# Kernel optimization log

Hardware: AMD Instinct MI355X
Metric: run time of the kernel (lower is better)

Reference implementation:

```python
import jax, jax.numpy as jnp
import numpy as np
import math

B, S, H, Dh, Dr, HID, C = 2, 2048, 16, 128, 64, 2048, 512

def _linear(x, w, b):
    return x @ w.T + b

def _rope(x):
    # x: [B, H, S, Dr]; interleaved-pair rotation as in the torch module
    d = x.shape[-1]
    s = x.shape[2]
    inv_freq = 1.0 / (10000.0 ** (jnp.arange(0, d, 2, dtype=jnp.float32) / d))
    sinusoid = jnp.arange(s, dtype=jnp.float32)[:, None] * inv_freq[None, :]  # [S, d/2]
    sin, cos = jnp.sin(sinusoid), jnp.cos(sinusoid)  # broadcast over B,H
    x1 = x[..., 0::2]
    x2 = x[..., 1::2]
    rot = jnp.stack([x1 * cos - x2 * sin, x1 * sin + x2 * cos], axis=-1)
    return rot.reshape(x.shape)

def setup_inputs() -> dict:
    key = jax.random.key(0)
    ks = jax.random.split(key, 9)
    sc = 0.02
    return {
        "x": jax.random.normal(ks[0], (B, S, HID), jnp.float32),
        "d_kv_w": jax.random.normal(ks[1], (C, HID), jnp.float32) * sc,
        "d_kv_b": jnp.zeros((C,), jnp.float32),
        "u_k_w": jax.random.normal(ks[2], (H * Dh, C), jnp.float32) * sc,
        "u_k_b": jnp.zeros((H * Dh,), jnp.float32),
        "u_v_w": jax.random.normal(ks[3], (H * Dh, C), jnp.float32) * sc,
        "u_v_b": jnp.zeros((H * Dh,), jnp.float32),
        "d_q_w": jax.random.normal(ks[4], (C, HID), jnp.float32) * sc,
        "d_q_b": jnp.zeros((C,), jnp.float32),
        "u_q_w": jax.random.normal(ks[5], (H * Dh, C), jnp.float32) * sc,
        "u_q_b": jnp.zeros((H * Dh,), jnp.float32),
        "qr_w": jax.random.normal(ks[6], (H * Dr, C), jnp.float32) * sc,
        "qr_b": jnp.zeros((H * Dr,), jnp.float32),
        "out_w": jax.random.normal(ks[7], (HID, H * Dh), jnp.float32) * sc,
        "out_b": jnp.zeros((HID,), jnp.float32),
    }

def reference(x, d_kv_w, d_kv_b, u_k_w, u_k_b, u_v_w, u_v_b,
              d_q_w, d_q_b, u_q_w, u_q_b, qr_w, qr_b, out_w, out_b):
    b, s, _ = x.shape
    kv_c = _linear(x, d_kv_w, d_kv_b)                      # [B,S,C]
    k_c = _linear(kv_c, u_k_w, u_k_b).reshape(b, s, H, Dh)
    k_r = _linear(kv_c, qr_w, qr_b).reshape(b, s, H, Dr)   # note: qr_proj reused, as in source
    v = _linear(kv_c, u_v_w, u_v_b).reshape(b, s, H, Dh)
    q_c_lat = _linear(x, d_q_w, d_q_b)                     # [B,S,C]
    q_c = _linear(q_c_lat, u_q_w, u_q_b).reshape(b, s, H, Dh)
    q_r = _linear(q_c_lat, qr_w, qr_b).reshape(b, s, H, Dr)
    # RoPE operates on [B,H,S,Dr]
    q_r = _rope(q_r.transpose(0, 2, 1, 3)).transpose(0, 2, 1, 3)
    k_r = _rope(k_r.transpose(0, 2, 1, 3)).transpose(0, 2, 1, 3)
    q = jnp.concatenate([q_c, q_r], axis=-1)               # [B,S,H,Dh+Dr]
    k = jnp.concatenate([k_c, k_r], axis=-1)
    scale = 1.0 / math.sqrt(Dh + Dr)
    scores = jnp.einsum('bqhd,bkhd->bhqk', q, k) * scale   # [B,H,S,S]
    probs = jax.nn.softmax(scores, axis=-1)
    ctx = jnp.einsum('bhqk,bkhd->bqhd', probs, v).reshape(b, s, H * Dh)
    return _linear(ctx, out_w, out_b)
```

## Files before the change

### kernel.cpp

```cpp
#include <hip/hip_runtime.h>
#include <hip/hip_bf16.h>
#include <math.h>
#include <stdint.h>

#define NB 2
#define NS 2048
#define NH 16
#define NDH 128
#define NDR 64
#define NHID 2048
#define NC 512

typedef unsigned short u16;
typedef short short8 __attribute__((ext_vector_type(8)));
typedef short short4v __attribute__((ext_vector_type(4)));
typedef float f32x4 __attribute__((ext_vector_type(4)));
typedef float f32x16 __attribute__((ext_vector_type(16)));
typedef int int2v __attribute__((ext_vector_type(2)));

template <int V> struct IC { static constexpr int value = V; };

__device__ __forceinline__ u16 f2bf(float f) {
  union { float f; uint32_t u; } c; c.f = f;
  uint32_t u = c.u + 0x7fffu + ((c.u >> 16) & 1u);
  return (u16)(u >> 16);
}
__device__ __forceinline__ void async16(const void* g, void* l) {
  __builtin_amdgcn_global_load_lds((const __attribute__((address_space(1))) void*)g,
                                   (__attribute__((address_space(3))) void*)l, 16, 0, 0);
}
__device__ __forceinline__ int cvtpk(float a, float b) {
  int r;
  asm("v_cvt_pk_bf16_f32 %0, %1, %2" : "=v"(r) : "v"(a), "v"(b));
  return r;
}
__device__ __forceinline__ void fsincos(float ang, float& sn, float& cs) {
  float rev = ang * 0.15915494309189535f;
  rev = rev - floorf(rev);
  float s, c;
  asm("v_sin_f32 %0, %1" : "=v"(s) : "v"(rev));
  asm("v_cos_f32 %0, %1" : "=v"(c) : "v"(rev));
  sn = s; cs = c;
}

struct CastArgs {
  const float* src[8];
  u16* dst[8];
  int start[8];
};

__global__ __launch_bounds__(256) void cast_kernel(CastArgs a) {
  int blk = blockIdx.x;
  int ti = 0;
#pragma unroll
  for (int i = 1; i < 8; ++i) ti += (blk >= a.start[i]) ? 1 : 0;
  size_t off = (size_t)(blk - a.start[ti]) * 2048 + (size_t)threadIdx.x * 8;
  const float4* s = (const float4*)(a.src[ti] + off);
  float4 v0 = s[0], v1 = s[1];
  u16 o[8];
  o[0] = f2bf(v0.x); o[1] = f2bf(v0.y); o[2] = f2bf(v0.z); o[3] = f2bf(v0.w);
  o[4] = f2bf(v1.x); o[5] = f2bf(v1.y); o[6] = f2bf(v1.z); o[7] = f2bf(v1.w);
  *(short8*)(a.dst[ti] + off) = *(short8*)o;
}

struct GemmSeg {
  const u16* A;
  const u16* W;
  const float* bias;
  void* dst;
  int K;
  int mode;
  int ldc;
};
struct GemmArgs {
  GemmSeg seg[5];
  int nbstart[6];
  int nseg;
};

template <int NW>
__global__ __launch_bounds__(NW * 64) void gemm_bt(GemmArgs ga) {
  constexpr int NT = NW * 64;
  constexpr int NJ = (NW == 8) ? 2 : 4;
  __shared__ char glds[32768];
  const int nb = blockIdx.x, mb = blockIdx.y;
  int si = 0;
  for (int i = 1; i < ga.nseg; ++i) si += (nb >= ga.nbstart[i]) ? 1 : 0;
  GemmSeg sg = ga.seg[si];
  const int nbl = nb - ga.nbstart[si];
  const int K = sg.K;
  const int t = threadIdx.x;
  const int l = t & 63, w = t >> 6;
  const int r0 = t >> 2, c0 = (t & 3) * 8;
  const int wm = (NW == 8 ? (w >> 2) : (w >> 1)) * 64;
  const int wn = (NW == 8) ? (w & 3) * 32 : (w & 1) * 64;
  const int frow = l & 15, fk = (l >> 4) * 8;
  const int lafO = ((wm + frow) * 32 + fk) * 2;
  const int lbfO = 8192 + ((wn + frow) * 32 + fk) * 2;

  const u16* apA = sg.A + (size_t)mb * 128 * K + (size_t)r0 * K + c0;
  const u16* wpA = sg.W + (size_t)nbl * 128 * K + (size_t)r0 * K + c0;

  auto stage = [&](int bufOff) {
    if constexpr (NT == 512) {
      async16(apA, glds + bufOff + t * 16);
      async16(wpA, glds + bufOff + 8192 + t * 16);
    } else {
      async16(apA, glds + bufOff + t * 16);
      async16(apA + (size_t)64 * K, glds + bufOff + 4096 + t * 16);
      async16(wpA, glds + bufOff + 8192 + t * 16);
      async16(wpA + (size_t)64 * K, glds + bufOff + 12288 + t * 16);
    }
    apA += 32; wpA += 32;
  };

  const f32x4 vzero = {0.f, 0.f, 0.f, 0.f};
  f32x4 acc[4][NJ];
#pragma unroll
  for (int i = 0; i < 4; ++i)
#pragma unroll
    for (int j = 0; j < NJ; ++j) acc[i][j] = vzero;

  stage(0);
  const int nk = K / 32;

  auto ktile = [&](auto bufc, bool stageNext) {
    constexpr int BO = decltype(bufc)::value;
    if (stageNext) {
      stage(BO ^ 16384);
      if constexpr (NT == 512)
        asm volatile("s_waitcnt vmcnt(2)" ::: "memory");
      else
        asm volatile("s_waitcnt vmcnt(4)" ::: "memory");
    } else {
      asm volatile("s_waitcnt vmcnt(0)" ::: "memory");
    }
    __builtin_amdgcn_s_barrier();
    asm volatile("" ::: "memory");
    short8 af[4], bfr[NJ];
#pragma unroll
    for (int i = 0; i < 4; ++i) af[i] = *(const short8*)(glds + BO + lafO + i * 1024);
#pragma unroll
    for (int j = 0; j < NJ; ++j) bfr[j] = *(const short8*)(glds + BO + lbfO + j * 1024);
    __builtin_amdgcn_s_setprio(1);
#pragma unroll
    for (int i = 0; i < 4; ++i)
#pragma unroll
      for (int j = 0; j < NJ; ++j)
        acc[i][j] = __builtin_amdgcn_mfma_f32_16x16x32_bf16(af[i], bfr[j], acc[i][j], 0, 0, 0);
    __builtin_amdgcn_s_setprio(0);
    asm volatile("s_waitcnt lgkmcnt(0)" ::: "memory");
    __builtin_amdgcn_s_barrier();
  };

  for (int kk = 0; kk < nk; kk += 2) {
    ktile(IC<0>{}, true);
    ktile(IC<16384>{}, kk + 2 < nk);
  }

  const int rb = (l >> 4) * 4;
  const int cl = l & 15;
  const int mode = sg.mode;
  if (mode == 0) {
    u16* D = (u16*)sg.dst;
#pragma unroll
    for (int i = 0; i < 4; ++i)
#pragma unroll
      for (int j = 0; j < NJ; ++j) {
        int col = nbl * 128 + wn + j * 16 + cl;
        float bv = sg.bias[col];
#pragma unroll
        for (int r = 0; r < 4; ++r) {
          int row = mb * 128 + wm + i * 16 + rb + r;
          D[(size_t)row * sg.ldc + col] = f2bf(acc[i][j][r] + bv);
        }
      }
  } else if (mode == 2) {
    float* D = (float*)sg.dst;
#pragma unroll
    for (int i = 0; i < 4; ++i)
#pragma unroll
      for (int j = 0; j < NJ; ++j) {
        int col = nbl * 128 + wn + j * 16 + cl;
        float bv = sg.bias[col];
#pragma unroll
        for (int r = 0; r < 4; ++r) {
          int row = mb * 128 + wm + i * 16 + rb + r;
          D[(size_t)row * sg.ldc + col] = acc[i][j][r] + bv;
        }
      }
  } else if (mode == 1) {
    u16* D = (u16*)sg.dst;
#pragma unroll
    for (int i = 0; i < 4; ++i) {
      int row0 = mb * 128 + wm + i * 16 + rb;
      int bb = row0 >> 11, s = row0 & (NS - 1);
#pragma unroll
      for (int j = 0; j < NJ; ++j) {
        int col = nbl * 128 + wn + j * 16 + cl;
        int hh = col >> 7, dv = col & 127;
        float bv = sg.bias[col];
        u16 pk[4];
#pragma unroll
        for (int r = 0; r < 4; ++r) pk[r] = f2bf(acc[i][j][r] + bv);
        size_t cell = ((size_t)((bb * NH + hh) * (NS / 8) + (s >> 3)) * 128 + dv) * 8 + (s & 7);
        *(short4v*)(D + cell) = *(short4v*)pk;
      }
    }
  } else if (mode == 4) {
    u16* D = (u16*)sg.dst;
#pragma unroll
    for (int i = 0; i < 4; ++i) {
      int row0 = mb * 128 + wm + i * 16 + rb;
      int bb = row0 >> 11, s = row0 & (NS - 1);
#pragma unroll
      for (int j = 0; j < NJ; ++j) {
        int col = nbl * 128 + wn + j * 16 + cl;
        int hh = col >> 7, d = col & 127;
        float bv = sg.bias[col];
        size_t base = ((size_t)((bb * NH + hh) * 24 + (d >> 3)) * NS + s) * 8 + (d & 7);
#pragma unroll
        for (int r = 0; r < 4; ++r) D[base + r * 8] = f2bf(acc[i][j][r] + bv);
      }
    }
  } else if (mode == 5) {
    u16* D = (u16*)sg.dst;
#pragma unroll
    for (int i = 0; i < 4; ++i) {
      int row0 = mb * 128 + wm + i * 16 + rb;
      int bb = row0 >> 11, s = row0 & (NS - 1);
#pragma unroll
      for (int j = 0; j < NJ; ++j) {
        int col = nbl * 128 + wn + j * 16 + cl;
        int hh = col >> 6, dr = col & 63;
        int jp = dr >> 1;
        bool ev = !(dr & 1);
        float invf = exp2f(-(float)jp * 0.41524101186f);
        float bv = sg.bias[col];
        size_t base = ((size_t)((bb * NH + hh) * 24 + 16 + (dr >> 3)) * NS + s) * 8 + (dr & 7);
#pragma unroll
        for (int r = 0; r < 4; ++r) {
          float v = acc[i][j][r] + bv;
          float p = __shfl_xor(v, 1);
          float sn, cs;
          fsincos((float)(s + r) * invf, sn, cs);
          float out = ev ? (v * cs - p * sn) : (p * sn + v * cs);
          D[base + r * 8] = f2bf(out);
        }
      }
    }
  } else {
    u16* D = (u16*)sg.dst;
#pragma unroll
    for (int i = 0; i < 4; ++i) {
      int row0 = mb * 128 + wm + i * 16 + rb;
      int s = row0 & (NS - 1);
#pragma unroll
      for (int j = 0; j < NJ; ++j) {
        int col = nbl * 128 + wn + j * 16 + cl;
        int dr = col & 63;
        int jp = dr >> 1;
        bool ev = !(dr & 1);
        float invf = exp2f(-(float)jp * 0.41524101186f);
        float bv = sg.bias[col];
#pragma unroll
        for (int r = 0; r < 4; ++r) {
          float v = acc[i][j][r] + bv;
          float p = __shfl_xor(v, 1);
          float sn, cs;
          fsincos((float)(s + r) * invf, sn, cs);
          float out = ev ? (v * cs - p * sn) : (p * sn + v * cs);
          D[(size_t)(row0 + r) * sg.ldc + col] = f2bf(out);
        }
      }
    }
  }
}

__global__ __launch_bounds__(256, 2) void attn_kernel(
    const u16* __restrict__ Qc, const u16* __restrict__ Qr,
    const u16* __restrict__ Ktb, const u16* __restrict__ Vtb,
    u16* __restrict__ Ctx) {
  extern __shared__ char smem[];
  const int t = threadIdx.x, w = t >> 6, l = t & 63;
  const int hi = l >> 5, q32 = l & 31;
  const int lin = blockIdx.x;
  const int xcd = lin & 7, idx = lin >> 3;
  const int bh = xcd * 4 + (idx >> 4);
  const int qb = idx & 15;
  const int b = bh >> 4, h = bh & 15;
  const int q0 = qb * 128 + w * 32;

  short8 qf[12];
  {
    const u16* qcp = Qc + ((size_t)(b * NS + q0 + q32)) * NHID + h * NDH + hi * 8;
    const u16* qrp = Qr + ((size_t)(b * NS + q0 + q32)) * (NH * NDR) + h * NDR + hi * 8;
#pragma unroll
    for (int dw = 0; dw < 8; ++dw) qf[dw] = *(const short8*)(qcp + dw * 16);
#pragma unroll
    for (int dw = 0; dw < 4; ++dw) qf[8 + dw] = *(const short8*)(qrp + dw * 16);
  }
#pragma unroll
  for (int dw = 0; dw < 12; ++dw) asm volatile("" :: "v"(qf[dw]));

  const int w2 = t >> 6;
  const u16* kp[6];
#pragma unroll
  for (int r = 0; r < 6; ++r)
    kp[r] = Ktb + ((size_t)(bh * 24 + r * 4 + w2) * NS + l) * 8;
  const u16* vp = Vtb + (size_t)bh * NS * 128 + t * 8;

  const int kbase = q32 * 16 + hi * 1024;
  const int vbase = 24576 + q32 * 16 + hi * 2048;

  float lsum = 0.f;
  f32x16 acc[4];
#pragma unroll
  for (int i = 0; i < 4; ++i)
#pragma unroll
    for (int r = 0; r < 16; ++r) acc[i][r] = 0.f;
  const float scale2 = 0.10411757f;

  auto stage_into = [&](int bufOff) {
#pragma unroll
    for (int r = 0; r < 6; ++r) { async16(kp[r], smem + bufOff + r * 4096 + t * 16); kp[r] += 512; }
#pragma unroll
    for (int r = 0; r < 4; ++r) async16(vp + r * 2048, smem + bufOff + 24576 + r * 4096 + t * 16);
    vp += 8192;
  };
  stage_into(0);

  auto pv_block = [&](const f32x16& sp, int n, const char* base) {
#pragma unroll
    for (int w2i = 0; w2i < 2; ++w2i) {
      const int bse = w2i * 8;
      int A0 = cvtpk(sp[bse + 0], sp[bse + 1]);
      int A1 = cvtpk(sp[bse + 2], sp[bse + 3]);
      int B0 = cvtpk(sp[bse + 4], sp[bse + 5]);
      int B1 = cvtpk(sp[bse + 6], sp[bse + 7]);
      int2v r02 = __builtin_amdgcn_permlane32_swap(A0, B0, false, false);
      int2v r13 = __builtin_amdgcn_permlane32_swap(A1, B1, false, false);
      union { int i[4]; short8 s; } F;
      F.i[0] = r02[0]; F.i[1] = r13[0]; F.i[2] = r02[1]; F.i[3] = r13[1];
      const int W = n * 2 + w2i;
      __builtin_amdgcn_s_setprio(1);
#pragma unroll
      for (int d32 = 0; d32 < 4; ++d32) {
        short8 va = *(const short8*)(base + W * 4096 + d32 * 512);
        acc[d32] = __builtin_amdgcn_mfma_f32_32x32x16_bf16(va, F.s, acc[d32], 0, 0, 0);
      }
      __builtin_amdgcn_s_setprio(0);
    }
  };

  auto tile = [&](auto bufc, bool stageNext) {
    constexpr int BO = decltype(bufc)::value;
    if (stageNext) {
      stage_into(BO ^ 40960);
      asm volatile("s_waitcnt vmcnt(10)" ::: "memory");
    } else {
      asm volatile("s_waitcnt vmcnt(0)" ::: "memory");
    }
    __builtin_amdgcn_s_barrier();
    asm volatile("" ::: "memory");

    f32x16 sa0, sa1;
#pragma unroll
    for (int r = 0; r < 16; ++r) { sa0[r] = 0.f; sa1[r] = 0.f; }
#pragma unroll
    for (int dw = 0; dw < 12; ++dw) {
      short8 k0 = *(const short8*)(smem + BO + kbase + dw * 2048);
      __builtin_amdgcn_s_setprio(1);
      sa0 = __builtin_amdgcn_mfma_f32_32x32x16_bf16(k0, qf[dw], sa0, 0, 0, 0);
      __builtin_amdgcn_s_setprio(0);
    }
#pragma unroll
    for (int dw = 0; dw < 12; ++dw) {
      short8 k1 = *(const short8*)(smem + BO + kbase + dw * 2048 + 512);
      __builtin_amdgcn_s_setprio(1);
      sa1 = __builtin_amdgcn_mfma_f32_32x32x16_bf16(k1, qf[dw], sa1, 0, 0, 0);
      __builtin_amdgcn_s_setprio(0);
    }
    float ps = 0.f;
#pragma unroll
    for (int r = 0; r < 16; ++r) {
      float p = exp2f(sa0[r] * scale2);
      sa0[r] = p;
      ps += p;
    }
    pv_block(sa0, 0, (const char*)smem + BO + vbase);
#pragma unroll
    for (int r = 0; r < 16; ++r) {
      float p = exp2f(sa1[r] * scale2);
      sa1[r] = p;
      ps += p;
    }
    pv_block(sa1, 1, (const char*)smem + BO + vbase);
    ps += __shfl_xor(ps, 32);
    lsum += ps;

    asm volatile("s_waitcnt lgkmcnt(0)" ::: "memory");
    __builtin_amdgcn_s_barrier();
  };

  for (int kv = 0; kv < NS / 64; kv += 2) {
    tile(IC<0>{}, true);
    tile(IC<40960>{}, kv + 2 < NS / 64);
  }

  float invq = 1.f / lsum;
  u16* dst = Ctx + ((size_t)(b * NS + q0 + q32)) * NHID + h * NDH + hi * 4;
#pragma unroll
  for (int d32 = 0; d32 < 4; ++d32)
#pragma unroll
    for (int m2x = 0; m2x < 4; ++m2x) {
      float a0 = acc[d32][m2x * 4 + 0] * invq, a1 = acc[d32][m2x * 4 + 1] * invq;
      float a2 = acc[d32][m2x * 4 + 2] * invq, a3 = acc[d32][m2x * 4 + 3] * invq;
      union { int i[2]; short4v s; } pu;
      pu.i[0] = cvtpk(a0, a1);
      pu.i[1] = cvtpk(a2, a3);
      *(short4v*)(dst + d32 * 32 + m2x * 8) = pu.s;
    }
}

extern "C" void kernel_launch(void* const* d_in, const int* in_sizes, int n_in,
                              void* d_out, int out_size, void* d_ws, size_t ws_size,
                              hipStream_t stream) {
  (void)in_sizes; (void)n_in; (void)out_size;
  const float* x      = (const float*)d_in[0];
  const float* d_kv_w = (const float*)d_in[1];
  const float* d_kv_b = (const float*)d_in[2];
  const float* u_k_w  = (const float*)d_in[3];
  const float* u_k_b  = (const float*)d_in[4];
  const float* u_v_w  = (const float*)d_in[5];
  const float* u_v_b  = (const float*)d_in[6];
  const float* d_q_w  = (const float*)d_in[7];
  const float* d_q_b  = (const float*)d_in[8];
  const float* u_q_w  = (const float*)d_in[9];
  const float* u_q_b  = (const float*)d_in[10];
  const float* qr_w   = (const float*)d_in[11];
  const float* qr_b   = (const float*)d_in[12];
  const float* out_w  = (const float*)d_in[13];
  const float* out_b  = (const float*)d_in[14];

  char* ws = (char*)d_ws;
  size_t off = 0;
  auto alloc = [&](size_t bytes) -> void* {
    void* p = ws + off;
    off += (bytes + 255) & ~(size_t)255;
    return p;
  };
  u16* xb   = (u16*)alloc((size_t)NB * NS * NHID * 2);
  u16* wdkv = (u16*)alloc((size_t)NC * NHID * 2);
  u16* wuk  = (u16*)alloc((size_t)NH * NDH * NC * 2);
  u16* wuv  = (u16*)alloc((size_t)NH * NDH * NC * 2);
  u16* wdq  = (u16*)alloc((size_t)NC * NHID * 2);
  u16* wuq  = (u16*)alloc((size_t)NH * NDH * NC * 2);
  u16* wqr  = (u16*)alloc((size_t)NH * NDR * NC * 2);
  u16* wout = (u16*)alloc((size_t)NHID * NH * NDH * 2);
  u16* kvc  = (u16*)alloc((size_t)NB * NS * NC * 2);
  u16* qlat = (u16*)alloc((size_t)NB * NS * NC * 2);
  u16* Ktb  = (u16*)alloc((size_t)NB * NH * 24 * NS * 8 * 2);
  u16* Vtb  = (u16*)alloc((size_t)NB * NH * NS * NDH * 2);
  u16* Qc   = (u16*)alloc((size_t)NB * NS * NH * NDH * 2);
  u16* Qrt  = (u16*)alloc((size_t)NB * NS * NH * NDR * 2);
  u16* ctx  = xb;
  if (off > ws_size) return;

  {
    CastArgs ca;
    const float* srcs[8] = {x, d_kv_w, u_k_w, u_v_w, d_q_w, u_q_w, qr_w, out_w};
    u16* dsts[8] = {xb, wdkv, wuk, wuv, wdq, wuq, wqr, wout};
    int sizes[8] = {NB * NS * NHID, NC * NHID, NH * NDH * NC, NH * NDH * NC,
                    NC * NHID, NH * NDH * NC, NH * NDR * NC, NHID * NH * NDH};
    int st = 0;
    for (int i = 0; i < 8; ++i) {
      ca.src[i] = srcs[i]; ca.dst[i] = dsts[i]; ca.start[i] = st;
      st += sizes[i] / 2048;
    }
    cast_kernel<<<dim3(st), dim3(256), 0, stream>>>(ca);
  }

  {
    GemmArgs ga;
    ga.nseg = 2;
    ga.seg[0] = {xb, wdkv, d_kv_b, kvc, NHID, 0, NC};
    ga.seg[1] = {xb, wdq,  d_q_b,  qlat, NHID, 0, NC};
    for (int i = 2; i < 5; ++i) ga.seg[i] = ga.seg[0];
    ga.nbstart[0] = 0; ga.nbstart[1] = 4; ga.nbstart[2] = 8;
    ga.nbstart[3] = 8; ga.nbstart[4] = 8; ga.nbstart[5] = 8;
    gemm_bt<8><<<dim3(8, 32), dim3(512), 0, stream>>>(ga);
  }

  {
    GemmArgs ga;
    ga.nseg = 5;
    ga.seg[0] = {kvc,  wuk, u_k_b, Ktb, NC, 4, 0};
    ga.seg[1] = {kvc,  wuv, u_v_b, Vtb, NC, 1, 0};
    ga.seg[2] = {kvc,  wqr, qr_b,  Ktb, NC, 5, 0};
    ga.seg[3] = {qlat, wuq, u_q_b, Qc,  NC, 0, NH * NDH};
    ga.seg[4] = {qlat, wqr, qr_b,  Qrt, NC, 3, NH * NDR};
    ga.nbstart[0] = 0;  ga.nbstart[1] = 16; ga.nbstart[2] = 32;
    ga.nbstart[3] = 40; ga.nbstart[4] = 56; ga.nbstart[5] = 64;
    gemm_bt<4><<<dim3(64, 32), dim3(256), 0, stream>>>(ga);
  }

  hipFuncSetAttribute((const void*)attn_kernel,
                      hipFuncAttributeMaxDynamicSharedMemorySize, 81920);
  attn_kernel<<<dim3(512), dim3(256), 81920, stream>>>(Qc, Qrt, Ktb, Vtb, ctx);

  {
    GemmArgs ga;
    ga.nseg = 1;
    ga.seg[0] = {ctx, wout, out_b, d_out, NHID, 2, NHID};
    for (int i = 1; i < 5; ++i) ga.seg[i] = ga.seg[0];
    ga.nbstart[0] = 0;
    for (int i = 1; i < 6; ++i) ga.nbstart[i] = 16;
    gemm_bt<4><<<dim3(16, 32), dim3(256), 0, stream>>>(ga);
  }
}
```

Before: 256.0 us.

## Widen GEMM tiles, fold softmax scale into Q, row-sum via MFMA

```diff
diff --git a/kernel.cpp b/kernel.cpp
--- a/kernel.cpp
+++ b/kernel.cpp
@@ -17,6 +17,8 @@
 typedef float f32x4 __attribute__((ext_vector_type(4)));
 typedef float f32x16 __attribute__((ext_vector_type(16)));
 typedef int int2v __attribute__((ext_vector_type(2)));
+
+#define SC2 0.10411757f
 
 template <int V> struct IC { static constexpr int value = V; };
 
@@ -71,6 +73,7 @@
   int K;
   int mode;
   int ldc;
+  float oscale;
 };
 struct GemmArgs {
   GemmSeg seg[5];
@@ -78,11 +81,12 @@
   int nseg;
 };
 
-template <int NW>
-__global__ __launch_bounds__(NW * 64) void gemm_bt(GemmArgs ga) {
-  constexpr int NT = NW * 64;
-  constexpr int NJ = (NW == 8) ? 2 : 4;
-  __shared__ char glds[32768];
+template <int BN>
+__global__ __launch_bounds__(512) void gemm_bt(GemmArgs ga) {
+  constexpr int NT = 512;
+  constexpr int NJ = BN / 64;
+  constexpr int BUF = 8192 + BN * 64;
+  __shared__ char glds[2 * BUF];
   const int nb = blockIdx.x, mb = blockIdx.y;
   int si = 0;
   for (int i = 1; i < ga.nseg; ++i) si += (nb >= ga.nbstart[i]) ? 1 : 0;
@@ -92,25 +96,20 @@
   const int t = threadIdx.x;
   const int l = t & 63, w = t >> 6;
   const int r0 = t >> 2, c0 = (t & 3) * 8;
-  const int wm = (NW == 8 ? (w >> 2) : (w >> 1)) * 64;
-  const int wn = (NW == 8) ? (w & 3) * 32 : (w & 1) * 64;
+  const int wm = (w >> 2) * 64;
+  const int wn = (w & 3) * (BN / 4);
   const int frow = l & 15, fk = (l >> 4) * 8;
   const int lafO = ((wm + frow) * 32 + fk) * 2;
   const int lbfO = 8192 + ((wn + frow) * 32 + fk) * 2;
 
   const u16* apA = sg.A + (size_t)mb * 128 * K + (size_t)r0 * K + c0;
-  const u16* wpA = sg.W + (size_t)nbl * 128 * K + (size_t)r0 * K + c0;
+  const u16* wpA = sg.W + (size_t)nbl * BN * K + (size_t)r0 * K + c0;
 
   auto stage = [&](int bufOff) {
-    if constexpr (NT == 512) {
-      async16(apA, glds + bufOff + t * 16);
-      async16(wpA, glds + bufOff + 8192 + t * 16);
-    } else {
-      async16(apA, glds + bufOff + t * 16);
-      async16(apA + (size_t)64 * K, glds + bufOff + 4096 + t * 16);
-      async16(wpA, glds + bufOff + 8192 + t * 16);
-      async16(wpA + (size_t)64 * K, glds + bufOff + 12288 + t * 16);
-    }
+    async16(apA, glds + bufOff + t * 16);
+    async16(wpA, glds + bufOff + 8192 + t * 16);
+    if constexpr (BN == 256)
+      async16(wpA + (size_t)128 * K, glds + bufOff + 16384 + t * 16);
     apA += 32; wpA += 32;
   };
 
@@ -127,11 +126,11 @@
   auto ktile = [&](auto bufc, bool stageNext) {
     constexpr int BO = decltype(bufc)::value;
     if (stageNext) {
-      stage(BO ^ 16384);
-      if constexpr (NT == 512)
+      stage(BO ^ BUF);
+      if constexpr (BN == 256)
+        asm volatile("s_waitcnt vmcnt(3)" ::: "memory");
+      else
         asm volatile("s_waitcnt vmcnt(2)" ::: "memory");
-      else
-        asm volatile("s_waitcnt vmcnt(4)" ::: "memory");
     } else {
       asm volatile("s_waitcnt vmcnt(0)" ::: "memory");
     }
@@ -155,7 +154,7 @@
 
   for (int kk = 0; kk < nk; kk += 2) {
     ktile(IC<0>{}, true);
-    ktile(IC<16384>{}, kk + 2 < nk);
+    ktile(IC<BUF>{}, kk + 2 < nk);
   }
 
   const int rb = (l >> 4) * 4;
@@ -163,16 +162,17 @@
   const int mode = sg.mode;
   if (mode == 0) {
     u16* D = (u16*)sg.dst;
+    float os = sg.oscale;
 #pragma unroll
     for (int i = 0; i < 4; ++i)
 #pragma unroll
       for (int j = 0; j < NJ; ++j) {
-        int col = nbl * 128 + wn + j * 16 + cl;
+        int col = nbl * BN + wn + j * 16 + cl;
         float bv = sg.bias[col];
 #pragma unroll
         for (int r = 0; r < 4; ++r) {
           int row = mb * 128 + wm + i * 16 + rb + r;
-          D[(size_t)row * sg.ldc + col] = f2bf(acc[i][j][r] + bv);
+          D[(size_t)row * sg.ldc + col] = f2bf((acc[i][j][r] + bv) * os);
         }
       }
   } else if (mode == 2) {
@@ -181,7 +181,7 @@
     for (int i = 0; i < 4; ++i)
 #pragma unroll
       for (int j = 0; j < NJ; ++j) {
-        int col = nbl * 128 + wn + j * 16 + cl;
+        int col = nbl * BN + wn + j * 16 + cl;
         float bv = sg.bias[col];
 #pragma unroll
         for (int r = 0; r < 4; ++r) {
@@ -197,7 +197,7 @@
       int bb = row0 >> 11, s = row0 & (NS - 1);
 #pragma unroll
       for (int j = 0; j < NJ; ++j) {
-        int col = nbl * 128 + wn + j * 16 + cl;
+        int col = nbl * BN + wn + j * 16 + cl;
         int hh = col >> 7, dv = col & 127;
         float bv = sg.bias[col];
         u16 pk[4];
@@ -215,7 +215,7 @@
       int bb = row0 >> 11, s = row0 & (NS - 1);
 #pragma unroll
       for (int j = 0; j < NJ; ++j) {
-        int col = nbl * 128 + wn + j * 16 + cl;
+        int col = nbl * BN + wn + j * 16 + cl;
         int hh = col >> 7, d = col & 127;
         float bv = sg.bias[col];
         size_t base = ((size_t)((bb * NH + hh) * 24 + (d >> 3)) * NS + s) * 8 + (d & 7);
@@ -231,7 +231,7 @@
       int bb = row0 >> 11, s = row0 & (NS - 1);
 #pragma unroll
       for (int j = 0; j < NJ; ++j) {
-        int col = nbl * 128 + wn + j * 16 + cl;
+        int col = nbl * BN + wn + j * 16 + cl;
         int hh = col >> 6, dr = col & 63;
         int jp = dr >> 1;
         bool ev = !(dr & 1);
@@ -251,13 +251,14 @@
     }
   } else {
     u16* D = (u16*)sg.dst;
+    float os = sg.oscale;
 #pragma unroll
     for (int i = 0; i < 4; ++i) {
       int row0 = mb * 128 + wm + i * 16 + rb;
       int s = row0 & (NS - 1);
 #pragma unroll
       for (int j = 0; j < NJ; ++j) {
-        int col = nbl * 128 + wn + j * 16 + cl;
+        int col = nbl * BN + wn + j * 16 + cl;
         int dr = col & 63;
         int jp = dr >> 1;
         bool ev = !(dr & 1);
@@ -270,7 +271,7 @@
           float sn, cs;
           fsincos((float)(s + r) * invf, sn, cs);
           float out = ev ? (v * cs - p * sn) : (p * sn + v * cs);
-          D[(size_t)(row0 + r) * sg.ldc + col] = f2bf(out);
+          D[(size_t)(row0 + r) * sg.ldc + col] = f2bf(out * os);
         }
       }
     }
@@ -313,13 +314,14 @@
   const int kbase = q32 * 16 + hi * 1024;
   const int vbase = 24576 + q32 * 16 + hi * 2048;
 
-  float lsum = 0.f;
-  f32x16 acc[4];
-#pragma unroll
-  for (int i = 0; i < 4; ++i)
-#pragma unroll
-    for (int r = 0; r < 16; ++r) acc[i][r] = 0.f;
-  const float scale2 = 0.10411757f;
+  f32x16 acc[4], accS, fz;
+#pragma unroll
+  for (int r = 0; r < 16; ++r) { fz[r] = 0.f; accS[r] = 0.f; }
+#pragma unroll
+  for (int i = 0; i < 4; ++i) acc[i] = fz;
+  union { int i[4]; short8 s; } ONES;
+  ONES.i[0] = 0x3F803F80; ONES.i[1] = 0x3F803F80;
+  ONES.i[2] = 0x3F803F80; ONES.i[3] = 0x3F803F80;
 
   auto stage_into = [&](int bufOff) {
 #pragma unroll
@@ -330,14 +332,18 @@
   };
   stage_into(0);
 
-  auto pv_block = [&](const f32x16& sp, int n, const char* base) {
+  auto pv_block = [&](const f32x16& s, int n, const char* vb) {
 #pragma unroll
     for (int w2i = 0; w2i < 2; ++w2i) {
       const int bse = w2i * 8;
-      int A0 = cvtpk(sp[bse + 0], sp[bse + 1]);
-      int A1 = cvtpk(sp[bse + 2], sp[bse + 3]);
-      int B0 = cvtpk(sp[bse + 4], sp[bse + 5]);
-      int B1 = cvtpk(sp[bse + 6], sp[bse + 7]);
+      float p0 = exp2f(s[bse + 0]), p1 = exp2f(s[bse + 1]);
+      float p2 = exp2f(s[bse + 2]), p3 = exp2f(s[bse + 3]);
+      float p4 = exp2f(s[bse + 4]), p5 = exp2f(s[bse + 5]);
+      float p6 = exp2f(s[bse + 6]), p7 = exp2f(s[bse + 7]);
+      int A0 = cvtpk(p0, p1);
+      int A1 = cvtpk(p2, p3);
+      int B0 = cvtpk(p4, p5);
+      int B1 = cvtpk(p6, p7);
       int2v r02 = __builtin_amdgcn_permlane32_swap(A0, B0, false, false);
       int2v r13 = __builtin_amdgcn_permlane32_swap(A1, B1, false, false);
       union { int i[4]; short8 s; } F;
@@ -346,9 +352,10 @@
       __builtin_amdgcn_s_setprio(1);
 #pragma unroll
       for (int d32 = 0; d32 < 4; ++d32) {
-        short8 va = *(const short8*)(base + W * 4096 + d32 * 512);
+        short8 va = *(const short8*)(vb + W * 4096 + d32 * 512);
         acc[d32] = __builtin_amdgcn_mfma_f32_32x32x16_bf16(va, F.s, acc[d32], 0, 0, 0);
       }
+      accS = __builtin_amdgcn_mfma_f32_32x32x16_bf16(ONES.s, F.s, accS, 0, 0, 0);
       __builtin_amdgcn_s_setprio(0);
     }
   };
@@ -365,39 +372,27 @@
     asm volatile("" ::: "memory");
 
     f32x16 sa0, sa1;
-#pragma unroll
-    for (int r = 0; r < 16; ++r) { sa0[r] = 0.f; sa1[r] = 0.f; }
-#pragma unroll
-    for (int dw = 0; dw < 12; ++dw) {
+    {
+      short8 k0 = *(const short8*)(smem + BO + kbase);
+      short8 k1 = *(const short8*)(smem + BO + kbase + 512);
+      __builtin_amdgcn_s_setprio(1);
+      sa0 = __builtin_amdgcn_mfma_f32_32x32x16_bf16(k0, qf[0], fz, 0, 0, 0);
+      sa1 = __builtin_amdgcn_mfma_f32_32x32x16_bf16(k1, qf[0], fz, 0, 0, 0);
+      __builtin_amdgcn_s_setprio(0);
+    }
+#pragma unroll
+    for (int dw = 1; dw < 12; ++dw) {
       short8 k0 = *(const short8*)(smem + BO + kbase + dw * 2048);
+      short8 k1 = *(const short8*)(smem + BO + kbase + dw * 2048 + 512);
       __builtin_amdgcn_s_setprio(1);
       sa0 = __builtin_amdgcn_mfma_f32_32x32x16_bf16(k0, qf[dw], sa0, 0, 0, 0);
-      __builtin_amdgcn_s_setprio(0);
-    }
-#pragma unroll
-    for (int dw = 0; dw < 12; ++dw) {
-      short8 k1 = *(const short8*)(smem + BO + kbase + dw * 2048 + 512);
-      __builtin_amdgcn_s_setprio(1);
       sa1 = __builtin_amdgcn_mfma_f32_32x32x16_bf16(k1, qf[dw], sa1, 0, 0, 0);
       __builtin_amdgcn_s_setprio(0);
     }
-    float ps = 0.f;
-#pragma unroll
-    for (int r = 0; r < 16; ++r) {
-      float p = exp2f(sa0[r] * scale2);
-      sa0[r] = p;
-      ps += p;
-    }
-    pv_block(sa0, 0, (const char*)smem + BO + vbase);
-#pragma unroll
-    for (int r = 0; r < 16; ++r) {
-      float p = exp2f(sa1[r] * scale2);
-      sa1[r] = p;
-      ps += p;
-    }
-    pv_block(sa1, 1, (const char*)smem + BO + vbase);
-    ps += __shfl_xor(ps, 32);
-    lsum += ps;
+
+    const char* vb = (const char*)smem + BO + vbase;
+    pv_block(sa0, 0, vb);
+    pv_block(sa1, 1, vb);
 
     asm volatile("s_waitcnt lgkmcnt(0)" ::: "memory");
     __builtin_amdgcn_s_barrier();
@@ -408,7 +403,7 @@
     tile(IC<40960>{}, kv + 2 < NS / 64);
   }
 
-  float invq = 1.f / lsum;
+  float invq = 1.f / accS[0];
   u16* dst = Ctx + ((size_t)(b * NS + q0 + q32)) * NHID + h * NDH + hi * 4;
 #pragma unroll
   for (int d32 = 0; d32 < 4; ++d32)
@@ -484,25 +479,25 @@
   {
     GemmArgs ga;
     ga.nseg = 2;
-    ga.seg[0] = {xb, wdkv, d_kv_b, kvc, NHID, 0, NC};
-    ga.seg[1] = {xb, wdq,  d_q_b,  qlat, NHID, 0, NC};
+    ga.seg[0] = {xb, wdkv, d_kv_b, kvc, NHID, 0, NC, 1.f};
+    ga.seg[1] = {xb, wdq,  d_q_b,  qlat, NHID, 0, NC, 1.f};
     for (int i = 2; i < 5; ++i) ga.seg[i] = ga.seg[0];
     ga.nbstart[0] = 0; ga.nbstart[1] = 4; ga.nbstart[2] = 8;
     ga.nbstart[3] = 8; ga.nbstart[4] = 8; ga.nbstart[5] = 8;
-    gemm_bt<8><<<dim3(8, 32), dim3(512), 0, stream>>>(ga);
+    gemm_bt<128><<<dim3(8, 32), dim3(512), 0, stream>>>(ga);
   }
 
   {
     GemmArgs ga;
     ga.nseg = 5;
-    ga.seg[0] = {kvc,  wuk, u_k_b, Ktb, NC, 4, 0};
-    ga.seg[1] = {kvc,  wuv, u_v_b, Vtb, NC, 1, 0};
-    ga.seg[2] = {kvc,  wqr, qr_b,  Ktb, NC, 5, 0};
-    ga.seg[3] = {qlat, wuq, u_q_b, Qc,  NC, 0, NH * NDH};
-    ga.seg[4] = {qlat, wqr, qr_b,  Qrt, NC, 3, NH * NDR};
-    ga.nbstart[0] = 0;  ga.nbstart[1] = 16; ga.nbstart[2] = 32;
-    ga.nbstart[3] = 40; ga.nbstart[4] = 56; ga.nbstart[5] = 64;
-    gemm_bt<4><<<dim3(64, 32), dim3(256), 0, stream>>>(ga);
+    ga.seg[0] = {kvc,  wuk, u_k_b, Ktb, NC, 4, 0, 1.f};
+    ga.seg[1] = {kvc,  wuv, u_v_b, Vtb, NC, 1, 0, 1.f};
+    ga.seg[2] = {kvc,  wqr, qr_b,  Ktb, NC, 5, 0, 1.f};
+    ga.seg[3] = {qlat, wuq, u_q_b, Qc,  NC, 0, NH * NDH, SC2};
+    ga.seg[4] = {qlat, wqr, qr_b,  Qrt, NC, 3, NH * NDR, SC2};
+    ga.nbstart[0] = 0;  ga.nbstart[1] = 8;  ga.nbstart[2] = 16;
+    ga.nbstart[3] = 20; ga.nbstart[4] = 28; ga.nbstart[5] = 32;
+    gemm_bt<256><<<dim3(32, 32), dim3(512), 0, stream>>>(ga);
   }
 
   hipFuncSetAttribute((const void*)attn_kernel,
@@ -512,10 +507,10 @@
   {
     GemmArgs ga;
     ga.nseg = 1;
-    ga.seg[0] = {ctx, wout, out_b, d_out, NHID, 2, NHID};
+    ga.seg[0] = {ctx, wout, out_b, d_out, NHID, 2, NHID, 1.f};
     for (int i = 1; i < 5; ++i) ga.seg[i] = ga.seg[0];
     ga.nbstart[0] = 0;
-    for (int i = 1; i < 6; ++i) ga.nbstart[i] = 16;
-    gemm_bt<4><<<dim3(16, 32), dim3(256), 0, stream>>>(ga);
-  }
-}
+    for (int i = 1; i < 6; ++i) ga.nbstart[i] = 8;
+    gemm_bt<256><<<dim3(8, 32), dim3(512), 0, stream>>>(ga);
+  }
+}
```

Measured after the change: 255.6 us. Within noise of the previous version (-0.2%).
